# Optimization experiments

Hardware: AMD Instinct MI355X
Metric: run time of the kernel (lower is better)

## Reference

```python
import jax, jax.numpy as jnp
import numpy as np

FILL = -1024.0


def setup_inputs() -> dict:
    key = jax.random.key(0)
    ks = jax.random.split(key, 8)
    B, Q, K, D, KD, VD = 4, 4096, 4096, 512, 64, 64
    s = 0.02  # small init scale for numeric sanity
    return {
        "x": jax.random.normal(ks[0], (B, Q, D), dtype=jnp.float32),
        "buffer": jax.random.normal(ks[1], (B, K, D), dtype=jnp.float32),
        "mask": jax.random.randint(ks[2], (B, Q, K), 0, 2) > 0,
        "Wq": jax.random.normal(ks[3], (KD, D), dtype=jnp.float32) * s,
        "bq": jnp.zeros((KD,), dtype=jnp.float32),
        "Wk": jax.random.normal(ks[4], (KD, D), dtype=jnp.float32) * s,
        "bk": jnp.zeros((KD,), dtype=jnp.float32),
        "Wv": jax.random.normal(ks[5], (VD, D), dtype=jnp.float32) * s,
        "bv": jnp.zeros((VD,), dtype=jnp.float32),
    }


def reference(x, buffer, mask, Wq, bq, Wk, bk, Wv, bv):
    key_dim = Wq.shape[0]
    query = x @ Wq.T + bq          # [B, Q, KD]
    keys = buffer @ Wk.T + bk      # [B, K, KD]
    vals = buffer @ Wv.T + bv      # [B, K, VD]
    logits = jnp.einsum('bqd,bkd->bqk', query, keys) / np.sqrt(key_dim).astype(np.float32)
    logits = jnp.where(mask, logits, FILL)
    # stable softmax (same math as exp(x - max) / sum)
    probs = jax.nn.softmax(logits, axis=-1)
    read = jnp.einsum('bqk,bkd->bqd', probs, vals)  # [B, Q, VD]
    return read
```

## Files before the change

kernel.cpp:

```cpp
#include <hip/hip_runtime.h>
#include <hip/hip_bf16.h>

typedef float f32x4 __attribute__((ext_vector_type(4)));
typedef __bf16 bf16x8 __attribute__((ext_vector_type(8)));

#define NB 4
#define NQ 4096
#define NK 4096
#define DIM 512
#define KD 64

__device__ inline bf16x8 load_cvt8(const float* __restrict__ p) {
    float4 f0 = *(const float4*)p;
    float4 f1 = *(const float4*)(p + 4);
    bf16x8 r;
    r[0] = (__bf16)f0.x; r[1] = (__bf16)f0.y; r[2] = (__bf16)f0.z; r[3] = (__bf16)f0.w;
    r[4] = (__bf16)f1.x; r[5] = (__bf16)f1.y; r[6] = (__bf16)f1.z; r[7] = (__bf16)f1.w;
    return r;
}

__global__ __launch_bounds__(256) void proj_q_kernel(
        const float* __restrict__ x, const float* __restrict__ W,
        const float* __restrict__ bias, __bf16* __restrict__ out) {
    const int tid = threadIdx.x;
    const int w = tid >> 6, l = tid & 63;
    const int lr = l & 15, lk = l >> 4;
    const long rowbase = (long)blockIdx.x * 128 + w * 32;

    f32x4 acc[2][4] = {};
    for (int kk = 0; kk < DIM; kk += 32) {
        bf16x8 a0 = load_cvt8(x + (rowbase + lr) * DIM + kk + lk * 8);
        bf16x8 a1 = load_cvt8(x + (rowbase + 16 + lr) * DIM + kk + lk * 8);
        bf16x8 bw[4];
#pragma unroll
        for (int nb = 0; nb < 4; nb++)
            bw[nb] = load_cvt8(W + (long)(nb * 16 + lr) * DIM + kk + lk * 8);
#pragma unroll
        for (int nb = 0; nb < 4; nb++) {
            acc[0][nb] = __builtin_amdgcn_mfma_f32_16x16x32_bf16(a0, bw[nb], acc[0][nb], 0, 0, 0);
            acc[1][nb] = __builtin_amdgcn_mfma_f32_16x16x32_bf16(a1, bw[nb], acc[1][nb], 0, 0, 0);
        }
    }
#pragma unroll
    for (int nb = 0; nb < 4; nb++) {
        const int col = nb * 16 + lr;
        const float bs = bias[col];
#pragma unroll
        for (int mi = 0; mi < 2; mi++)
#pragma unroll
            for (int i = 0; i < 4; i++) {
                long row = rowbase + mi * 16 + lk * 4 + i;
                out[row * KD + col] = (__bf16)(acc[mi][nb][i] + bs);
            }
    }
}

__global__ __launch_bounds__(256) void proj_kv_kernel(
        const float* __restrict__ buf,
        const float* __restrict__ Wk, const float* __restrict__ bk,
        const float* __restrict__ Wv, const float* __restrict__ bv,
        __bf16* __restrict__ Kb, __bf16* __restrict__ Vt) {
    const int tid = threadIdx.x;
    const int w = tid >> 6, l = tid & 63;
    const int lr = l & 15, lk = l >> 4;
    const long rowbase = (long)blockIdx.x * 128 + w * 32;

    f32x4 acck[2][4] = {};
    f32x4 accv[2][4] = {};
    for (int kk = 0; kk < DIM; kk += 32) {
        bf16x8 a0 = load_cvt8(buf + (rowbase + lr) * DIM + kk + lk * 8);
        bf16x8 a1 = load_cvt8(buf + (rowbase + 16 + lr) * DIM + kk + lk * 8);
        bf16x8 bwk[4], bwv[4];
#pragma unroll
        for (int nb = 0; nb < 4; nb++) {
            bwk[nb] = load_cvt8(Wk + (long)(nb * 16 + lr) * DIM + kk + lk * 8);
            bwv[nb] = load_cvt8(Wv + (long)(nb * 16 + lr) * DIM + kk + lk * 8);
        }
#pragma unroll
        for (int nb = 0; nb < 4; nb++) {
            acck[0][nb] = __builtin_amdgcn_mfma_f32_16x16x32_bf16(a0, bwk[nb], acck[0][nb], 0, 0, 0);
            acck[1][nb] = __builtin_amdgcn_mfma_f32_16x16x32_bf16(a1, bwk[nb], acck[1][nb], 0, 0, 0);
            accv[0][nb] = __builtin_amdgcn_mfma_f32_16x16x32_bf16(a0, bwv[nb], accv[0][nb], 0, 0, 0);
            accv[1][nb] = __builtin_amdgcn_mfma_f32_16x16x32_bf16(a1, bwv[nb], accv[1][nb], 0, 0, 0);
        }
    }
#pragma unroll
    for (int nb = 0; nb < 4; nb++) {
        const int col = nb * 16 + lr;
        const float bsk = bk[col];
        const float bsv = bv[col];
#pragma unroll
        for (int mi = 0; mi < 2; mi++)
#pragma unroll
            for (int i = 0; i < 4; i++) {
                long row = rowbase + mi * 16 + lk * 4 + i;
                Kb[row * KD + col] = (__bf16)(acck[mi][nb][i] + bsk);
                int bidx = (int)(row >> 12);
                int kidx = (int)(row & 4095);
                Vt[((long)bidx * KD + col) * NK + kidx] = (__bf16)(accv[mi][nb][i] + bsv);
            }
    }
}

__global__ __launch_bounds__(256) void attn_kernel(
        const __bf16* __restrict__ Qb, const __bf16* __restrict__ Kb,
        const __bf16* __restrict__ Vt, const int* __restrict__ mask,
        float* __restrict__ out) {
    __shared__ __bf16 plds[4][16][72];

    const int tid = threadIdx.x;
    const int w = tid >> 6, l = tid & 63;
    const int lr = l & 15, lk = l >> 4;
    const int b = blockIdx.x >> 6;
    const int q0 = (blockIdx.x & 63) * 64 + w * 16;

    const __bf16* Qp = Qb + ((long)b * NQ + q0) * KD;
    const __bf16* Kp = Kb + (long)b * NK * KD;
    const __bf16* Vp = Vt + (long)b * KD * NK;
    const int*    mp = mask + ((long)b * NQ + q0) * NK;

    bf16x8 qa[2];
#pragma unroll
    for (int ks = 0; ks < 2; ks++)
        qa[ks] = *(const bf16x8*)(Qp + (long)lr * KD + ks * 32 + lk * 8);

    f32x4 o[4] = {};
    float m_i[4], l_i[4];
#pragma unroll
    for (int i = 0; i < 4; i++) { m_i[i] = -INFINITY; l_i[i] = 0.f; }

    for (int kt = 0; kt < NK; kt += 64) {
        f32x4 s[4] = {};
#pragma unroll
        for (int ks = 0; ks < 2; ks++)
#pragma unroll
            for (int nb = 0; nb < 4; nb++) {
                bf16x8 kb = *(const bf16x8*)(Kp + (long)(kt + nb * 16 + lr) * KD + ks * 32 + lk * 8);
                s[nb] = __builtin_amdgcn_mfma_f32_16x16x32_bf16(qa[ks], kb, s[nb], 0, 0, 0);
            }
#pragma unroll
        for (int nb = 0; nb < 4; nb++)
#pragma unroll
            for (int i = 0; i < 4; i++) {
                int mv = mp[(long)(lk * 4 + i) * NK + kt + nb * 16 + lr];
                s[nb][i] = mv ? s[nb][i] * 0.125f : -1024.0f;
            }
#pragma unroll
        for (int i = 0; i < 4; i++) {
            float v = fmaxf(fmaxf(s[0][i], s[1][i]), fmaxf(s[2][i], s[3][i]));
            v = fmaxf(v, __shfl_xor(v, 1));
            v = fmaxf(v, __shfl_xor(v, 2));
            v = fmaxf(v, __shfl_xor(v, 4));
            v = fmaxf(v, __shfl_xor(v, 8));
            float mnew = fmaxf(m_i[i], v);
            float sc = __expf(m_i[i] - mnew);
            m_i[i] = mnew;
            float rs = 0.f;
#pragma unroll
            for (int nb = 0; nb < 4; nb++) {
                float p = __expf(s[nb][i] - mnew);
                s[nb][i] = p;
                rs += p;
            }
            rs += __shfl_xor(rs, 1);
            rs += __shfl_xor(rs, 2);
            rs += __shfl_xor(rs, 4);
            rs += __shfl_xor(rs, 8);
            l_i[i] = l_i[i] * sc + rs;
#pragma unroll
            for (int nb = 0; nb < 4; nb++) o[nb][i] *= sc;
        }
#pragma unroll
        for (int nb = 0; nb < 4; nb++)
#pragma unroll
            for (int i = 0; i < 4; i++)
                plds[w][lk * 4 + i][nb * 16 + lr] = (__bf16)s[nb][i];
#pragma unroll
        for (int ks = 0; ks < 2; ks++) {
            bf16x8 pa = *(const bf16x8*)&plds[w][lr][ks * 32 + lk * 8];
#pragma unroll
            for (int nb = 0; nb < 4; nb++) {
                bf16x8 vb = *(const bf16x8*)(Vp + (long)(nb * 16 + lr) * NK + kt + ks * 32 + lk * 8);
                o[nb] = __builtin_amdgcn_mfma_f32_16x16x32_bf16(pa, vb, o[nb], 0, 0, 0);
            }
        }
    }
#pragma unroll
    for (int nb = 0; nb < 4; nb++)
#pragma unroll
        for (int i = 0; i < 4; i++) {
            long row = (long)b * NQ + q0 + lk * 4 + i;
            out[row * KD + nb * 16 + lr] = o[nb][i] / l_i[i];
        }
}

extern "C" void kernel_launch(void* const* d_in, const int* in_sizes, int n_in,
                              void* d_out, int out_size, void* d_ws, size_t ws_size,
                              hipStream_t stream) {
    const float* x      = (const float*)d_in[0];
    const float* buffer = (const float*)d_in[1];
    const int*   mask   = (const int*)d_in[2];
    const float* Wq     = (const float*)d_in[3];
    const float* bq     = (const float*)d_in[4];
    const float* Wk     = (const float*)d_in[5];
    const float* bk     = (const float*)d_in[6];
    const float* Wv     = (const float*)d_in[7];
    const float* bv     = (const float*)d_in[8];
    float* out = (float*)d_out;

    __bf16* Qb = (__bf16*)d_ws;
    __bf16* Kb = Qb + (size_t)NB * NQ * KD;
    __bf16* Vt = Kb + (size_t)NB * NK * KD;

    proj_q_kernel<<<dim3((NB * NQ) / 128), dim3(256), 0, stream>>>(x, Wq, bq, Qb);
    proj_kv_kernel<<<dim3((NB * NK) / 128), dim3(256), 0, stream>>>(buffer, Wk, bk, Wv, bv, Kb, Vt);
    attn_kernel<<<dim3(NB * (NQ / 64)), dim3(256), 0, stream>>>(Qb, Kb, Vt, mask, out);
}
```

Baseline: 279.8 us.

## Split attention over key dimension across waves and merge projection kernels

The attention kernel now gives each block 16 query rows and splits the 4096 keys across 8 waves, with 512 keys per wave. The partial softmax states are then combined through LDS with a log-sum-exp merge. This raises the block count and the number of in-flight mask loads per query row. The old grid of 256 blocks left MI355X CUs underused. The Q and K/V projections are fused into one launch with split-K across waves and an LDS reduction, which also gives coalesced Vt transposed stores. The cost is extra LDS traffic, two syncthreads per block and merge arithmetic.

```diff
diff --git a/kernel.cpp b/kernel.cpp
--- a/kernel.cpp
+++ b/kernel.cpp
@@ -19,106 +19,99 @@
     return r;
 }
 
-__global__ __launch_bounds__(256) void proj_q_kernel(
-        const float* __restrict__ x, const float* __restrict__ W,
-        const float* __restrict__ bias, __bf16* __restrict__ out) {
+__global__ __launch_bounds__(256, 4) void proj_kernel(
+        const float* __restrict__ x, const float* __restrict__ buf,
+        const float* __restrict__ Wq, const float* __restrict__ bq,
+        const float* __restrict__ Wk, const float* __restrict__ bk,
+        const float* __restrict__ Wv, const float* __restrict__ bv,
+        __bf16* __restrict__ Qb, __bf16* __restrict__ Kb, __bf16* __restrict__ Vt) {
+    __shared__ __align__(16) float ps[4][32][66];
+
     const int tid = threadIdx.x;
     const int w = tid >> 6, l = tid & 63;
     const int lr = l & 15, lk = l >> 4;
-    const long rowbase = (long)blockIdx.x * 128 + w * 32;
-
-    f32x4 acc[2][4] = {};
-    for (int kk = 0; kk < DIM; kk += 32) {
-        bf16x8 a0 = load_cvt8(x + (rowbase + lr) * DIM + kk + lk * 8);
-        bf16x8 a1 = load_cvt8(x + (rowbase + 16 + lr) * DIM + kk + lk * 8);
-        bf16x8 bw[4];
-#pragma unroll
-        for (int nb = 0; nb < 4; nb++)
-            bw[nb] = load_cvt8(W + (long)(nb * 16 + lr) * DIM + kk + lk * 8);
-#pragma unroll
-        for (int nb = 0; nb < 4; nb++) {
-            acc[0][nb] = __builtin_amdgcn_mfma_f32_16x16x32_bf16(a0, bw[nb], acc[0][nb], 0, 0, 0);
-            acc[1][nb] = __builtin_amdgcn_mfma_f32_16x16x32_bf16(a1, bw[nb], acc[1][nb], 0, 0, 0);
-        }
-    }
-#pragma unroll
-    for (int nb = 0; nb < 4; nb++) {
-        const int col = nb * 16 + lr;
-        const float bs = bias[col];
-#pragma unroll
-        for (int mi = 0; mi < 2; mi++)
+    const int rg = w >> 1, kh = w & 1;
+    const bool is_q = blockIdx.x < 512;
+    const int blk = is_q ? blockIdx.x : blockIdx.x - 512;
+    const long rowbase = (long)blk * 32 + rg * 16;
+    const int kbase = kh * 256;
+
+    if (is_q) {
+        f32x4 acc[4] = {};
+        for (int kk = 0; kk < 256; kk += 32) {
+            bf16x8 a = load_cvt8(x + (rowbase + lr) * DIM + kbase + kk + lk * 8);
+#pragma unroll
+            for (int nb = 0; nb < 4; nb++) {
+                bf16x8 bw = load_cvt8(Wq + (long)(nb * 16 + lr) * DIM + kbase + kk + lk * 8);
+                acc[nb] = __builtin_amdgcn_mfma_f32_16x16x32_bf16(a, bw, acc[nb], 0, 0, 0);
+            }
+        }
+#pragma unroll
+        for (int nb = 0; nb < 4; nb++)
+#pragma unroll
+            for (int i = 0; i < 4; i++)
+                ps[kh * 2][rg * 16 + lk * 4 + i][nb * 16 + lr] = acc[nb][i];
+        __syncthreads();
+        for (int e = tid; e < 2048; e += 256) {
+            int row = e >> 6, col = e & 63;
+            float v = ps[0][row][col] + ps[2][row][col] + bq[col];
+            Qb[((long)blk * 32 + row) * KD + col] = (__bf16)v;
+        }
+    } else {
+        f32x4 acck[4] = {}, accv[4] = {};
+        for (int kk = 0; kk < 256; kk += 32) {
+            bf16x8 a = load_cvt8(buf + (rowbase + lr) * DIM + kbase + kk + lk * 8);
+#pragma unroll
+            for (int nb = 0; nb < 4; nb++) {
+                bf16x8 bwk = load_cvt8(Wk + (long)(nb * 16 + lr) * DIM + kbase + kk + lk * 8);
+                bf16x8 bwv = load_cvt8(Wv + (long)(nb * 16 + lr) * DIM + kbase + kk + lk * 8);
+                acck[nb] = __builtin_amdgcn_mfma_f32_16x16x32_bf16(a, bwk, acck[nb], 0, 0, 0);
+                accv[nb] = __builtin_amdgcn_mfma_f32_16x16x32_bf16(a, bwv, accv[nb], 0, 0, 0);
+            }
+        }
+#pragma unroll
+        for (int nb = 0; nb < 4; nb++)
 #pragma unroll
             for (int i = 0; i < 4; i++) {
-                long row = rowbase + mi * 16 + lk * 4 + i;
-                out[row * KD + col] = (__bf16)(acc[mi][nb][i] + bs);
-            }
-    }
-}
-
-__global__ __launch_bounds__(256) void proj_kv_kernel(
-        const float* __restrict__ buf,
-        const float* __restrict__ Wk, const float* __restrict__ bk,
-        const float* __restrict__ Wv, const float* __restrict__ bv,
-        __bf16* __restrict__ Kb, __bf16* __restrict__ Vt) {
+                ps[kh * 2 + 0][rg * 16 + lk * 4 + i][nb * 16 + lr] = acck[nb][i];
+                ps[kh * 2 + 1][rg * 16 + lk * 4 + i][nb * 16 + lr] = accv[nb][i];
+            }
+        __syncthreads();
+        for (int e = tid; e < 2048; e += 256) {
+            int row = e >> 6, col = e & 63;
+            float v = ps[0][row][col] + ps[2][row][col] + bk[col];
+            Kb[((long)blk * 32 + row) * KD + col] = (__bf16)v;
+        }
+        for (int e = tid; e < 2048; e += 256) {
+            int row = e & 31, col = e >> 5;
+            float v = ps[1][row][col] + ps[3][row][col] + bv[col];
+            long grow = (long)blk * 32 + row;
+            int b = (int)(grow >> 12), kidx = (int)(grow & 4095);
+            Vt[((long)b * KD + col) * NK + kidx] = (__bf16)v;
+        }
+    }
+}
+
+__global__ __launch_bounds__(512, 8) void attn_kernel(
+        const __bf16* __restrict__ Qb, const __bf16* __restrict__ Kb,
+        const __bf16* __restrict__ Vt, const int* __restrict__ mask,
+        float* __restrict__ out) {
+    __shared__ __align__(16) char smem[8 * 16 * 66 * 4 + 8 * 2 * 16 * 4];
+
     const int tid = threadIdx.x;
     const int w = tid >> 6, l = tid & 63;
     const int lr = l & 15, lk = l >> 4;
-    const long rowbase = (long)blockIdx.x * 128 + w * 32;
-
-    f32x4 acck[2][4] = {};
-    f32x4 accv[2][4] = {};
-    for (int kk = 0; kk < DIM; kk += 32) {
-        bf16x8 a0 = load_cvt8(buf + (rowbase + lr) * DIM + kk + lk * 8);
-        bf16x8 a1 = load_cvt8(buf + (rowbase + 16 + lr) * DIM + kk + lk * 8);
-        bf16x8 bwk[4], bwv[4];
-#pragma unroll
-        for (int nb = 0; nb < 4; nb++) {
-            bwk[nb] = load_cvt8(Wk + (long)(nb * 16 + lr) * DIM + kk + lk * 8);
-            bwv[nb] = load_cvt8(Wv + (long)(nb * 16 + lr) * DIM + kk + lk * 8);
-        }
-#pragma unroll
-        for (int nb = 0; nb < 4; nb++) {
-            acck[0][nb] = __builtin_amdgcn_mfma_f32_16x16x32_bf16(a0, bwk[nb], acck[0][nb], 0, 0, 0);
-            acck[1][nb] = __builtin_amdgcn_mfma_f32_16x16x32_bf16(a1, bwk[nb], acck[1][nb], 0, 0, 0);
-            accv[0][nb] = __builtin_amdgcn_mfma_f32_16x16x32_bf16(a0, bwv[nb], accv[0][nb], 0, 0, 0);
-            accv[1][nb] = __builtin_amdgcn_mfma_f32_16x16x32_bf16(a1, bwv[nb], accv[1][nb], 0, 0, 0);
-        }
-    }
-#pragma unroll
-    for (int nb = 0; nb < 4; nb++) {
-        const int col = nb * 16 + lr;
-        const float bsk = bk[col];
-        const float bsv = bv[col];
-#pragma unroll
-        for (int mi = 0; mi < 2; mi++)
-#pragma unroll
-            for (int i = 0; i < 4; i++) {
-                long row = rowbase + mi * 16 + lk * 4 + i;
-                Kb[row * KD + col] = (__bf16)(acck[mi][nb][i] + bsk);
-                int bidx = (int)(row >> 12);
-                int kidx = (int)(row & 4095);
-                Vt[((long)bidx * KD + col) * NK + kidx] = (__bf16)(accv[mi][nb][i] + bsv);
-            }
-    }
-}
-
-__global__ __launch_bounds__(256) void attn_kernel(
-        const __bf16* __restrict__ Qb, const __bf16* __restrict__ Kb,
-        const __bf16* __restrict__ Vt, const int* __restrict__ mask,
-        float* __restrict__ out) {
-    __shared__ __bf16 plds[4][16][72];
-
-    const int tid = threadIdx.x;
-    const int w = tid >> 6, l = tid & 63;
-    const int lr = l & 15, lk = l >> 4;
-    const int b = blockIdx.x >> 6;
-    const int q0 = (blockIdx.x & 63) * 64 + w * 16;
+    const int b = blockIdx.x >> 8;
+    const int q0 = (blockIdx.x & 255) * 16;
+    const int k0 = w * 512;
 
     const __bf16* Qp = Qb + ((long)b * NQ + q0) * KD;
     const __bf16* Kp = Kb + (long)b * NK * KD;
     const __bf16* Vp = Vt + (long)b * KD * NK;
     const int*    mp = mask + ((long)b * NQ + q0) * NK;
 
+    __bf16 (*pl)[72] = (__bf16(*)[72])(smem + w * 2304);
+
     bf16x8 qa[2];
 #pragma unroll
     for (int ks = 0; ks < 2; ks++)
@@ -129,7 +122,7 @@
 #pragma unroll
     for (int i = 0; i < 4; i++) { m_i[i] = -INFINITY; l_i[i] = 0.f; }
 
-    for (int kt = 0; kt < NK; kt += 64) {
+    for (int kt = k0; kt < k0 + 512; kt += 64) {
         f32x4 s[4] = {};
 #pragma unroll
         for (int ks = 0; ks < 2; ks++)
@@ -174,10 +167,10 @@
         for (int nb = 0; nb < 4; nb++)
 #pragma unroll
             for (int i = 0; i < 4; i++)
-                plds[w][lk * 4 + i][nb * 16 + lr] = (__bf16)s[nb][i];
+                pl[lk * 4 + i][nb * 16 + lr] = (__bf16)s[nb][i];
 #pragma unroll
         for (int ks = 0; ks < 2; ks++) {
-            bf16x8 pa = *(const bf16x8*)&plds[w][lr][ks * 32 + lk * 8];
+            bf16x8 pa = *(const bf16x8*)&pl[lr][ks * 32 + lk * 8];
 #pragma unroll
             for (int nb = 0; nb < 4; nb++) {
                 bf16x8 vb = *(const bf16x8*)(Vp + (long)(nb * 16 + lr) * NK + kt + ks * 32 + lk * 8);
@@ -185,13 +178,37 @@
             }
         }
     }
+
+    __syncthreads();
+    float* o_s = (float*)smem;
+    float* ml  = (float*)(smem + 8 * 16 * 66 * 4);
 #pragma unroll
     for (int nb = 0; nb < 4; nb++)
 #pragma unroll
+        for (int i = 0; i < 4; i++)
+            o_s[(w * 16 + lk * 4 + i) * 66 + nb * 16 + lr] = o[nb][i];
+    if (lr == 0) {
+#pragma unroll
         for (int i = 0; i < 4; i++) {
-            long row = (long)b * NQ + q0 + lk * 4 + i;
-            out[row * KD + nb * 16 + lr] = o[nb][i] / l_i[i];
-        }
+            ml[w * 32 + lk * 4 + i]      = m_i[i];
+            ml[w * 32 + 16 + lk * 4 + i] = l_i[i];
+        }
+    }
+    __syncthreads();
+    for (int e = tid; e < 1024; e += 512) {
+        int row = e >> 6, col = e & 63;
+        float M = -INFINITY;
+#pragma unroll
+        for (int ww = 0; ww < 8; ww++) M = fmaxf(M, ml[ww * 32 + row]);
+        float L = 0.f, O = 0.f;
+#pragma unroll
+        for (int ww = 0; ww < 8; ww++) {
+            float f = __expf(ml[ww * 32 + row] - M);
+            L += f * ml[ww * 32 + 16 + row];
+            O += f * o_s[(ww * 16 + row) * 66 + col];
+        }
+        out[((long)b * NQ + q0 + row) * KD + col] = O / L;
+    }
 }
 
 extern "C" void kernel_launch(void* const* d_in, const int* in_sizes, int n_in,
@@ -212,7 +229,6 @@
     __bf16* Kb = Qb + (size_t)NB * NQ * KD;
     __bf16* Vt = Kb + (size_t)NB * NK * KD;
 
-    proj_q_kernel<<<dim3((NB * NQ) / 128), dim3(256), 0, stream>>>(x, Wq, bq, Qb);
-    proj_kv_kernel<<<dim3((NB * NK) / 128), dim3(256), 0, stream>>>(buffer, Wk, bk, Wv, bv, Kb, Vt);
-    attn_kernel<<<dim3(NB * (NQ / 64)), dim3(256), 0, stream>>>(Qb, Kb, Vt, mask, out);
-}
+    proj_kernel<<<dim3(1024), dim3(256), 0, stream>>>(x, buffer, Wq, bq, Wk, bk, Wv, bv, Qb, Kb, Vt);
+    attn_kernel<<<dim3(NB * (NQ / 16)), dim3(512), 0, stream>>>(Qb, Kb, Vt, mask, out);
+}
```

Measured after the change: 377.2 us. 1.35x slower.
